# Kernel tuning notes

Measured on AMD Instinct MI355X. Metric: run time of the kernel, lower is better.

The kernel has to match this reference:

```python
import jax, jax.numpy as jnp
import numpy as np

N, E, G = 8192, 65536, 16          # nodes, edges, graphs
EMBED, HID, L = 512, 1024, 3       # embed_dim, hidden_dim, hidden_layers
NG, RBF_R = 50, 12.0               # num_gaussians, rbf_radius
AVG_LEN = 60.0
IN_DIM = 3 * EMBED


def _mlp_params(key, in_dim, hid, out_dim, n_layers):
    ks = jax.random.split(key, 6)
    s_in = 1.0 / np.sqrt(in_dim)
    s_h = 1.0 / np.sqrt(hid)
    return dict(
        in_w=jax.random.normal(ks[0], (in_dim, hid), jnp.float32) * s_in,
        in_b=jnp.zeros((hid,), jnp.float32),
        hid_w=jax.random.normal(ks[1], (n_layers, hid, hid), jnp.float32) * s_h,
        hid_b=jnp.zeros((n_layers, hid), jnp.float32),
        out_w=jax.random.normal(ks[2], (hid, out_dim), jnp.float32) * s_h,
        out_b=jnp.zeros((out_dim,), jnp.float32),
    )


def setup_inputs() -> dict:
    key = jax.random.key(0)
    k = jax.random.split(key, 8)
    x = jax.random.normal(k[0], (N, EMBED), jnp.float32)
    edge_index = jax.random.randint(k[1], (2, E), 0, N, dtype=jnp.int32)
    batch = jnp.sort(jax.random.randint(k[2], (N,), 0, G, dtype=jnp.int32))
    dist = jax.random.uniform(k[3], (E,), jnp.float32) * RBF_R
    v = jax.random.normal(k[4], (E, 3), jnp.float32)
    vec_hat = v / jnp.linalg.norm(v, axis=-1, keepdims=True)
    rbf_w = jax.random.normal(k[5], (NG, EMBED), jnp.float32) * (1.0 / np.sqrt(NG))
    rbf_b = jnp.zeros((EMBED,), jnp.float32)
    e = _mlp_params(k[6], IN_DIM, HID, 1, L)
    f = _mlp_params(k[7], IN_DIM, HID, 1, L)
    return dict(
        x=x, edge_index=edge_index, batch=batch, dist=dist, vec_hat=vec_hat,
        rbf_w=rbf_w, rbf_b=rbf_b,
        e_in_w=e['in_w'], e_in_b=e['in_b'], e_hid_w=e['hid_w'], e_hid_b=e['hid_b'], e_out_w=e['out_w'], e_out_b=e['out_b'],
        f_in_w=f['in_w'], f_in_b=f['in_b'], f_hid_w=f['hid_w'], f_hid_b=f['hid_b'], f_out_w=f['out_w'], f_out_b=f['out_b'],
    )


def _res_mlp(h_in, in_w, in_b, hid_w, hid_b, out_w, out_b):
    h = jax.nn.silu(h_in @ in_w + in_b)           # [E, HID]
    for i in range(L):                             # residual hidden blocks
        h = h + jax.nn.silu(h @ hid_w[i] + hid_b[i])
    return h @ out_w + out_b                       # [E, 1]


def _rbf(dist, rbf_w, rbf_b):
    offsets = jnp.linspace(0.0, RBF_R, NG)
    coeff = -0.5 / (offsets[1] - offsets[0]) ** 2
    g = jnp.exp(coeff * (dist[:, None] - offsets) ** 2)  # [E, NG]
    return g @ rbf_w + rbf_b                              # [E, EMBED]


def reference(x, edge_index, batch, dist, vec_hat,
              rbf_w, rbf_b,
              e_in_w, e_in_b, e_hid_w, e_hid_b, e_out_w, e_out_b,
              f_in_w, f_in_b, f_hid_w, f_hid_b, f_out_w, f_out_b):
    src, dst = edge_index[0], edge_index[1]
    rbf = _rbf(dist, rbf_w, rbf_b)                                 # [E, EMBED]
    inputs = jnp.concatenate([x[src], x[dst], rbf], axis=-1)       # [E, 3*EMBED]
    energy_pairs = _res_mlp(inputs, e_in_w, e_in_b, e_hid_w, e_hid_b, e_out_w, e_out_b)  # [E,1]
    force_pairs = _res_mlp(inputs, f_in_w, f_in_b, f_hid_w, f_hid_b, f_out_w, f_out_b) * vec_hat  # [E,3]
    energy = jax.ops.segment_sum(energy_pairs, batch[src], num_segments=G) / (AVG_LEN ** 2)  # [G,1]
    forces = jax.ops.segment_sum(force_pairs, src, num_segments=N) / AVG_LEN                 # [N,3]
    return energy, forces
```

## Files before the change

kernel.cpp:

```cpp
#include <hip/hip_runtime.h>
#include <math.h>

#define NUM_E 65536
#define NUM_N 8192
#define NUM_G 16
#define RBFR 12.0f

typedef unsigned short u16;
typedef _Float16 f16x8 __attribute__((ext_vector_type(8)));
typedef _Float16 f16x4 __attribute__((ext_vector_type(4)));
typedef float f32x4 __attribute__((ext_vector_type(4)));

#define TILE_F16 4096
#define L1SZ   1114112
#define HSZ    1048576
#define MSTRIDE 4259840

#define FU1  139264
#define FUHL 131072
#define FUPM (FU1 + 3 * FUHL)

#define GLD16(gp, lp) __builtin_amdgcn_global_load_lds( \
    (const __attribute__((address_space(1))) void*)(gp), \
    (__attribute__((address_space(3))) void*)(lp), 16, 0, 0)

#define VMW3()  asm volatile("s_waitcnt vmcnt(3)" ::: "memory")
#define VMW0()  asm volatile("s_waitcnt vmcnt(0)" ::: "memory")
#define BARX()  __builtin_amdgcn_s_barrier()

__global__ void wrbf_kernel(const float* __restrict__ rbf_w, const float* __restrict__ rbf_b,
                            const float* __restrict__ e_in_w, const float* __restrict__ e_in_b,
                            const float* __restrict__ f_in_w, const float* __restrict__ f_in_b,
                            float* __restrict__ wrbf_e, float* __restrict__ b1_e,
                            float* __restrict__ wrbf_f, float* __restrict__ b1_f) {
  int blk = blockIdx.x;
  int mlp = blk / 204;
  int rr = blk % 204;
  int row = rr >> 2;
  int ns = rr & 3;
  const float* in_w = mlp ? f_in_w : e_in_w;
  const float* in_b = mlp ? f_in_b : e_in_b;
  float* wrbf = mlp ? wrbf_f : wrbf_e;
  float* b1   = mlp ? b1_f : b1_e;
  __shared__ float vec[512];
  __shared__ float4 red[256];
  int tid = threadIdx.x;
  vec[tid]       = (row < 50) ? rbf_w[row * 512 + tid]       : rbf_b[tid];
  vec[tid + 256] = (row < 50) ? rbf_w[row * 512 + tid + 256] : rbf_b[tid + 256];
  __syncthreads();
  int q = tid >> 6, l = tid & 63;
  int n0 = ns * 256 + l * 4;
  float a0 = 0.f, a1 = 0.f, a2 = 0.f, a3 = 0.f;
#pragma unroll 4
  for (int c = q * 128; c < q * 128 + 128; ++c) {
    float4 wv = *(const float4*)&in_w[(size_t)(1024 + c) * 1024 + n0];
    float gv = vec[c];
    a0 += gv * wv.x; a1 += gv * wv.y; a2 += gv * wv.z; a3 += gv * wv.w;
  }
  red[tid] = float4{a0, a1, a2, a3};
  __syncthreads();
  if (q == 0) {
    float4 s0 = red[l], s1 = red[l + 64], s2 = red[l + 128], s3 = red[l + 192];
    float4 o = {s0.x + s1.x + s2.x + s3.x, s0.y + s1.y + s2.y + s3.y,
                s0.z + s1.z + s2.z + s3.z, s0.w + s1.w + s2.w + s3.w};
    if (row < 50) {
      *(float4*)&wrbf[row * 1024 + n0] = o;
    } else {
      o.x += in_b[n0]; o.y += in_b[n0 + 1]; o.z += in_b[n0 + 2]; o.w += in_b[n0 + 3];
      *(float4*)&b1[n0] = o;
    }
  }
}

__global__ void prep_kernel(const float* __restrict__ x, const float* __restrict__ dist,
                            u16* __restrict__ xh, u16* __restrict__ grbf) {
  int bid = blockIdx.x, tid = threadIdx.x;
  if (bid < 4096) {
    int i = bid * 256 + tid;
    float4 v = ((const float4*)x)[i];
    f16x4 h = {(_Float16)v.x, (_Float16)v.y, (_Float16)v.z, (_Float16)v.w};
    *(f16x4*)(xh + (size_t)i * 4) = h;
  } else {
    int u = (bid - 4096) * 256 + tid;
    int e = u >> 3, q = u & 7;
    const float delta = RBFR / 49.f;
    const float coeff = -0.5f / (delta * delta);
    float d = dist[e];
    f16x8 h;
#pragma unroll
    for (int j = 0; j < 8; ++j) {
      int gi = q * 8 + j;
      float dd = d - (float)gi * delta;
      float gg = (gi < 50) ? __expf(coeff * dd * dd) : 0.f;
      h[j] = (_Float16)gg;
    }
    *(f16x8*)(grbf + (size_t)u * 8) = h;
  }
}

__global__ void pack_gemm(const float* __restrict__ e_in_w, const float* __restrict__ e_hid_w,
                          const float* __restrict__ f_in_w, const float* __restrict__ f_hid_w,
                          const float* __restrict__ wrbf_e, const float* __restrict__ wrbf_f,
                          u16* __restrict__ wp) {
  __shared__ __align__(16) u16 tile[TILE_F16];
  int bid = blockIdx.x;
  int mlpi = (bid >= 1040) ? 1 : 0;
  int t = bid - mlpi * 1040;
  const float* in_w  = mlpi ? f_in_w : e_in_w;
  const float* hid_w = mlpi ? f_hid_w : e_hid_w;
  const float* wrbf  = mlpi ? wrbf_f : wrbf_e;
  int tid = threadIdx.x;
  int bnp, nhp, k0, lay = 0, is_l1;
  if (t < 272) {
    int grp = t / 34; int kt = t % 34;
    bnp = grp >> 1; nhp = grp & 1; k0 = kt * 32; is_l1 = 1;
  } else {
    int th = t - 272; lay = th >> 8; int t2 = th & 255;
    bnp = t2 >> 6; nhp = (t2 >> 5) & 1; k0 = (t2 & 31) * 32; is_l1 = 0;
  }
#pragma unroll
  for (int it = 0; it < 4; ++it) {
    int flat = it * 1024 + tid * 4;
    int k = flat >> 7;
    int nl4 = flat & 127;
    int n0 = bnp * 256 + ((nl4 >> 5) << 6) + nhp * 32 + (nl4 & 31);
    int kg = k0 + k;
    float4 v;
    if (is_l1) {
      if (kg < 1024)      v = *(const float4*)&in_w[(size_t)kg * 1024 + n0];
      else if (kg < 1074) v = *(const float4*)&wrbf[(size_t)(kg - 1024) * 1024 + n0];
      else                v = float4{0.f, 0.f, 0.f, 0.f};
    } else {
      v = *(const float4*)&hid_w[(size_t)((lay << 10) + kg) * 1024 + n0];
    }
#pragma unroll
    for (int c = 0; c < 4; ++c) {
      int nl = nl4 + c;
      int pos = nl * 32 + (((((k >> 3) ^ ((nl >> 1) & 3))) << 3) | (k & 7));
      _Float16 hf = (_Float16)(((const float*)&v)[c]);
      tile[pos] = __builtin_bit_cast(u16, hf);
    }
  }
  __syncthreads();
  u16* dst = wp + (size_t)mlpi * MSTRIDE + (size_t)t * TILE_F16;
#pragma unroll
  for (int i = 0; i < 2; ++i) {
    int off = (i * 256 + tid) * 8;
    *(f16x8*)(dst + off) = *(const f16x8*)(tile + off);
  }
}


#define STA(b, ah, kt) do { \
  const u16* _gp; \
  if (MODE == 1) { \
    int _off = ((kt) < 16) ? (osrc[ah] + (kt) * 32) \
             : (((kt) < 32) ? (odst[ah] + ((kt) - 16) * 32) : (ogr[ah] + ((kt) - 32) * 32)); \
    _gp = (((kt) < 32) ? hin : grbf) + _off; \
  } else { \
    _gp = hin + ((size_t)(rowb + atr + (ah) * 32) * 1024 + (kt) * 32 + akg * 8); \
  } \
  GLD16(_gp, (char*)&sm[b][ah][0] + wv * 1024); \
} while (0)

#define STB(b, kt) do { \
  const u16* _wt = wl + ((size_t)(bn * NKT + (kt))) * TILE_F16; \
  GLD16(_wt + wv * 512 + lane * 8, (char*)&sm[b][2][0] + wv * 1024); \
} while (0)

#define RDA(b, ah) do { \
  _Pragma("unroll") for (int _m = 0; _m < 2; ++_m) { \
    int _r = wm * 32 + _m * 16 + (lane & 15); \
    af[_m] = *(const f16x8*)&sm[b][ah][_r * 32 + ((((lane >> 4) ^ ((_r >> 1) & 3))) << 3)]; \
  } \
} while (0)

#define RDB(b) do { \
  _Pragma("unroll") for (int _n = 0; _n < 4; ++_n) { \
    int _c = wn * 64 + _n * 16 + (lane & 15); \
    bf[_n] = *(const f16x8*)&sm[b][2][_c * 32 + ((((lane >> 4) ^ ((_c >> 1) & 3))) << 3)]; \
  } \
} while (0)

#define PHM(ah) do { \
  __builtin_amdgcn_s_setprio(1); \
  _Pragma("unroll") for (int _m = 0; _m < 2; ++_m) \
    _Pragma("unroll") for (int _n = 0; _n < 4; ++_n) \
      acc[(ah) * 2 + _m][_n] = __builtin_amdgcn_mfma_f32_16x16x32_f16( \
          bf[_n], af[_m], acc[(ah) * 2 + _m][_n], 0, 0, 0); \
  __builtin_amdgcn_s_setprio(0); \
} while (0)

template<int NKT, int MODE>
__global__ __launch_bounds__(512, 4) void gemm8k(
    const u16* __restrict__ hinE, const u16* __restrict__ hinF,
    const u16* __restrict__ grbf, const int* __restrict__ eidx,
    const int* __restrict__ batch, const float* __restrict__ vhat,
    const u16* __restrict__ wp, size_t woff,
    const float* __restrict__ biasE, const float* __restrict__ biasF,
    u16* __restrict__ houtE, u16* __restrict__ houtF,
    const float* __restrict__ owE, const float* __restrict__ owF,
    const float* __restrict__ obE, const float* __restrict__ obF,
    float* __restrict__ out, int mstart) {
  __shared__ __align__(16) u16 sm[2][3][4096];
  __shared__ int s_src[256];
  __shared__ int s_dst[256];
  __shared__ float sred[256];
  __shared__ float sbins[16];
  const int tid = threadIdx.x;
  const int lane = tid & 63;
  const int wv = tid >> 6;
  const int wm = wv >> 1, wn = wv & 1;

  const int xcd = blockIdx.x & 7;
  const int r = blockIdx.x >> 3;
  const int bn = r & 7;
  const int mlp = (r >> 3) & 1;
  const int mt = (r >> 4) * 8 + xcd;

  const u16* hin = (MODE == 1) ? hinE : (mlp ? hinF : hinE);
  const u16* wl = wp + (size_t)mlp * MSTRIDE + woff;
  const float* bias = mlp ? biasF : biasE;
  u16* hout = mlp ? houtF : houtE;
  const int rowb = mt * 256;
  const int eg0 = mstart + rowb;
  const int bnp = bn >> 1, nhp = bn & 1;

  const int arl = wv * 16 + (lane >> 2);
  const int akg = (lane & 3) ^ ((arl >> 1) & 3);
  const int atr = ((arl >> 5) << 6) + (arl & 31);

  int osrc[2], odst[2], ogr[2];
  if (MODE == 1) {
    if (tid < 256) s_src[tid] = eidx[eg0 + tid];
    else s_dst[tid - 256] = eidx[NUM_E + eg0 + tid - 256];
    __syncthreads();
#pragma unroll
    for (int ah = 0; ah < 2; ++ah) {
      int tr = atr + ah * 32;
      osrc[ah] = s_src[tr] * 512 + akg * 8;
      odst[ah] = s_dst[tr] * 512 + akg * 8;
      ogr[ah]  = (eg0 + tr) * 64 + akg * 8;
    }
  }

  f32x4 acc[4][4];
#pragma unroll
  for (int m = 0; m < 4; ++m)
#pragma unroll
    for (int n = 0; n < 4; ++n)
#pragma unroll
      for (int i = 0; i < 4; ++i) acc[m][n][i] = 0.f;

  f16x8 af[2], bf[4];

  STA(0, 0, 0); STB(0, 0); STA(0, 1, 0);
  VMW0(); BARX();

  for (int t = 0; t < NKT - 1; ++t) {
    const int b = t & 1, nb = b ^ 1;
    STA(nb, 0, t + 1); STB(nb, t + 1); STA(nb, 1, t + 1);
    VMW3(); BARX();
    RDA(b, 0); RDB(b);
    PHM(0);
    RDA(b, 1);
    PHM(1);
    BARX();
  }
  {
    const int tb = (NKT - 1) & 1;
    VMW0(); BARX();
    RDA(tb, 0); RDB(tb);
    PHM(0);
    RDA(tb, 1);
    PHM(1);
  }

  if (MODE != 2) {
#pragma unroll
    for (int m = 0; m < 4; ++m) {
      int grow = rowb + wm * 64 + (m >> 1) * 32 + (m & 1) * 16 + (lane & 15);
#pragma unroll
      for (int n = 0; n < 4; ++n) {
        int c = wn * 64 + n * 16 + ((lane >> 4) << 2);
        int gn = bnp * 256 + ((c >> 5) << 6) + nhp * 32 + (c & 31);
        float4 bi = *(const float4*)&bias[gn];
        f16x4 o;
        if (MODE == 1) {
#pragma unroll
          for (int i = 0; i < 4; ++i) {
            float pre = acc[m][n][i] + ((const float*)&bi)[i];
            o[i] = (_Float16)(pre / (1.f + __expf(-pre)));
          }
        } else {
          f16x4 hp = *(const f16x4*)&hin[(size_t)grow * 1024 + gn];
#pragma unroll
          for (int i = 0; i < 4; ++i) {
            float pre = acc[m][n][i] + ((const float*)&bi)[i];
            o[i] = (_Float16)(pre / (1.f + __expf(-pre)) + (float)hp[i]);
          }
        }
        *(f16x4*)&hout[(size_t)grow * 1024 + gn] = o;
      }
    }
  } else {
    if (tid < 256) sred[tid] = 0.f;
    if (tid < 16) sbins[tid] = 0.f;
    __syncthreads();
    const float* ow = mlp ? owF : owE;
    float p[4];
#pragma unroll
    for (int m = 0; m < 4; ++m) p[m] = 0.f;
#pragma unroll
    for (int m = 0; m < 4; ++m) {
      int grow = rowb + wm * 64 + (m >> 1) * 32 + (m & 1) * 16 + (lane & 15);
#pragma unroll
      for (int n = 0; n < 4; ++n) {
        int c = wn * 64 + n * 16 + ((lane >> 4) << 2);
        int gn = bnp * 256 + ((c >> 5) << 6) + nhp * 32 + (c & 31);
        float4 bi = *(const float4*)&bias[gn];
        float4 wv4 = *(const float4*)&ow[gn];
        f16x4 hp = *(const f16x4*)&hin[(size_t)grow * 1024 + gn];
#pragma unroll
        for (int i = 0; i < 4; ++i) {
          float pre = acc[m][n][i] + ((const float*)&bi)[i];
          float val = pre / (1.f + __expf(-pre)) + (float)hp[i];
          p[m] += val * ((const float*)&wv4)[i];
        }
      }
    }
#pragma unroll
    for (int m = 0; m < 4; ++m) {
      p[m] += __shfl_down(p[m], 32, 64);
      p[m] += __shfl_down(p[m], 16, 64);
    }
    if ((lane >> 4) == 0) {
#pragma unroll
      for (int m = 0; m < 4; ++m)
        atomicAdd(&sred[wm * 64 + (m >> 1) * 32 + (m & 1) * 16 + lane], p[m]);
    }
    __syncthreads();
    if (tid < 256) {
      float s = sred[tid];
      int eg = eg0 + tid;
      int si = eidx[eg];
      if (mlp == 0) {
        float pv = s + ((bn == 0) ? obE[0] : 0.f);
        atomicAdd(&sbins[batch[si]], pv);
      } else {
        float pv = (s + ((bn == 0) ? obF[0] : 0.f)) * (1.f / 60.f);
        atomicAdd(&out[16 + si * 3 + 0], pv * vhat[(size_t)eg * 3 + 0]);
        atomicAdd(&out[16 + si * 3 + 1], pv * vhat[(size_t)eg * 3 + 1]);
        atomicAdd(&out[16 + si * 3 + 2], pv * vhat[(size_t)eg * 3 + 2]);
      }
    }
    __syncthreads();
    if (mlp == 0 && tid < 16) atomicAdd(&out[tid], sbins[tid] * (1.f / 3600.f));
  }
}

#define FSWZ(row, col) ((((row) * 1088) + (col)) ^ (((row) & 7) << 3))

__global__ void packF_kernel(const float* __restrict__ e_in_w, const float* __restrict__ e_hid_w,
                             const float* __restrict__ f_in_w, const float* __restrict__ f_hid_w,
                             const float* __restrict__ wrbf_e, const float* __restrict__ wrbf_f,
                             u16* __restrict__ wp) {
  int u = blockIdx.x * 256 + threadIdx.x;
  if (u >= 2 * FUPM) return;
  int m = (u >= FUPM) ? 1 : 0;
  int v = u - m * FUPM;
  const float* in_w  = m ? f_in_w : e_in_w;
  const float* hid_w = m ? f_hid_w : e_hid_w;
  const float* wrbf  = m ? wrbf_f : wrbf_e;
  int l = v & 63;
  int kb = (l >> 4) << 3;
  f16x8 vals;
  if (v < FU1) {
    int kt = v >> 12;
    int ntg = (v >> 6) & 63;
    int n = ntg * 16 + (l & 15);
    int k0 = kt * 32 + kb;
#pragma unroll
    for (int jj = 0; jj < 8; ++jj) {
      int k = k0 + jj;
      float f = (k < 1024) ? in_w[(size_t)k * 1024 + n]
              : ((k < 1074) ? wrbf[(k - 1024) * 1024 + n] : 0.f);
      vals[jj] = (_Float16)f;
    }
  } else {
    int vh = v - FU1;
    int lay = vh >> 17;
    int kt = (vh >> 12) & 31;
    int ntg = (vh >> 6) & 63;
    int n = ntg * 16 + (l & 15);
    int k0 = kt * 32 + kb;
#pragma unroll
    for (int jj = 0; jj < 8; ++jj)
      vals[jj] = (_Float16)hid_w[(size_t)((lay << 10) + k0 + jj) * 1024 + n];
  }
  *(f16x8*)(wp + (size_t)u * 8) = vals;
}

#define F_LOADB(buf, kt) do { \
  const u16* _wr = wl + ((size_t)((kt) * 64 + wave * 8) * 64 + lane) * 8; \
  _Pragma("unroll") \
  for (int _nt = 0; _nt < 8; ++_nt) buf[_nt] = *(const f16x8*)(_wr + (size_t)_nt * 512); \
} while (0)
#define F_LOADA(buf, kt) do { \
  const int _kb = (kt) * 32 + ((lane >> 4) << 3); \
  _Pragma("unroll") \
  for (int _r = 0; _r < 4; ++_r) buf[_r] = *(const f16x8*)&Alds[FSWZ(_r * 16 + (lane & 15), _kb)]; \
} while (0)
#define F_MFMAS(abuf, bbuf) do { \
  _Pragma("unroll") \
  for (int _nt = 0; _nt < 8; ++_nt) \
    _Pragma("unroll") \
    for (int _r = 0; _r < 4; ++_r) \
      acc[_r][_nt] = __builtin_amdgcn_mfma_f32_16x16x32_f16(abuf[_r], bbuf[_nt], acc[_r][_nt], 0, 0, 0); \
} while (0)

__global__ __launch_bounds__(512, 2) void fusedF_kernel(
    const float* __restrict__ x, const int* __restrict__ eidx,
    const int* __restrict__ batch, const float* __restrict__ dist,
    const float* __restrict__ vhat,
    const u16* __restrict__ wp,
    const float* __restrict__ b1_e, const float* __restrict__ b1_f,
    const float* __restrict__ e_hid_b, const float* __restrict__ f_hid_b,
    const float* __restrict__ e_out_w, const float* __restrict__ e_out_b,
    const float* __restrict__ f_out_w, const float* __restrict__ f_out_b,
    float* __restrict__ out) {
  __shared__ __align__(16) u16 Alds[64 * 1088];
  __shared__ float sow[1024];
  __shared__ float sbins[16];
  __shared__ int s_src[64];
  __shared__ int s_dst[64];
  __shared__ float s_dist[64];
  const int tid = threadIdx.x;
  const int lane = tid & 63;
  const int wave = tid >> 6;
  const int e0 = blockIdx.x * 64;
  if (tid < 16) sbins[tid] = 0.f;
  if (tid < 64) s_src[tid] = eidx[e0 + tid];
  if (tid >= 64 && tid < 128) s_dst[tid - 64] = eidx[NUM_E + e0 + tid - 64];
  if (tid >= 128 && tid < 192) s_dist[tid - 128] = dist[e0 + tid - 128];
  __syncthreads();
  const float delta = RBFR / 49.f;
  const float coeff = -0.5f / (delta * delta);
  for (int mlp = 0; mlp < 2; ++mlp) {
    for (int i = tid; i < 16384; i += 512) {
      int e = i >> 8;
      int part = (i >> 7) & 1;
      int q = i & 127;
      int nrow = part ? s_dst[e] : s_src[e];
      float4 v = ((const float4*)x)[(size_t)nrow * 128 + q];
      int col = part * 512 + q * 4;
      f16x4 hv = {(_Float16)v.x, (_Float16)v.y, (_Float16)v.z, (_Float16)v.w};
      *(f16x4*)&Alds[FSWZ(e, col)] = hv;
    }
    for (int i = tid; i < 4096; i += 512) {
      int e = i >> 6;
      int gi = i & 63;
      float d = s_dist[e] - (float)gi * delta;
      float g2 = (gi < 50) ? __expf(coeff * d * d) : 0.f;
      _Float16 hg = (_Float16)g2;
      Alds[FSWZ(e, 1024 + gi)] = __builtin_bit_cast(u16, hg);
    }
    __syncthreads();
    const u16* wp1 = wp + (size_t)mlp * FUPM * 8;
    const u16* wph = wp1 + (size_t)FU1 * 8;
    const float* b1 = mlp ? b1_f : b1_e;
    const float* hb = mlp ? f_hid_b : e_hid_b;
    for (int layer = 0; layer < 4; ++layer) {
      const int nkt = (layer == 0) ? 34 : 32;
      const u16* wl = (layer == 0) ? wp1 : (wph + (size_t)(layer - 1) * FUHL * 8);
      const float* bias = (layer == 0) ? b1 : (hb + (layer - 1) * 1024);
      f32x4 acc[4][8];
#pragma unroll
      for (int r = 0; r < 4; ++r)
#pragma unroll
        for (int nt = 0; nt < 8; ++nt)
#pragma unroll
          for (int i = 0; i < 4; ++i) acc[r][nt][i] = 0.f;
      f16x8 a0[4], a1[4], b0[8], b1r[8];
      F_LOADA(a0, 0); F_LOADB(b0, 0);
      F_LOADA(a1, 1); F_LOADB(b1r, 1);
      for (int kt = 0; kt < nkt; kt += 2) {
        F_MFMAS(a0, b0);
        if (kt + 2 < nkt) { F_LOADA(a0, kt + 2); F_LOADB(b0, kt + 2); }
        F_MFMAS(a1, b1r);
        if (kt + 3 < nkt) { F_LOADA(a1, kt + 3); F_LOADB(b1r, kt + 3); }
      }
      __syncthreads();
      float bia[8];
#pragma unroll
      for (int nt = 0; nt < 8; ++nt) bia[nt] = bias[wave * 128 + nt * 16 + (lane & 15)];
#pragma unroll
      for (int r = 0; r < 4; ++r) {
#pragma unroll
        for (int nt = 0; nt < 8; ++nt) {
#pragma unroll
          for (int i = 0; i < 4; ++i) {
            int row = r * 16 + ((lane >> 4) << 2) + i;
            int col = wave * 128 + nt * 16 + (lane & 15);
            float pre = acc[r][nt][i] + bia[nt];
            float val = pre / (1.f + __expf(-pre));
            int idx = FSWZ(row, col);
            if (layer > 0) {
              _Float16 oldh = __builtin_bit_cast(_Float16, Alds[idx]);
              val += (float)oldh;
            }
            _Float16 nh = (_Float16)val;
            Alds[idx] = __builtin_bit_cast(u16, nh);
          }
        }
      }
      __syncthreads();
    }
    const float* ow = mlp ? f_out_w : e_out_w;
    for (int i = tid; i < 1024; i += 512) sow[i] = ow[i];
    __syncthreads();
    {
      int e = tid >> 3;
      int part = tid & 7;
      float s = 0.f;
#pragma unroll
      for (int cc = 0; cc < 16; ++cc) {
        int col = part * 128 + cc * 8;
        f16x8 hv = *(const f16x8*)&Alds[FSWZ(e, col)];
#pragma unroll
        for (int q = 0; q < 8; ++q) s += (float)hv[q] * sow[col + q];
      }
      s += __shfl_down(s, 4, 8);
      s += __shfl_down(s, 2, 8);
      s += __shfl_down(s, 1, 8);
      if (part == 0) {
        if (mlp == 0) {
          float pp = s + e_out_b[0];
          int gg = batch[s_src[e]];
          atomicAdd(&sbins[gg], pp);
        } else {
          float pp = (s + f_out_b[0]) * (1.f / 60.f);
          int si = s_src[e];
          atomicAdd(&out[16 + si * 3 + 0], pp * vhat[(size_t)(e0 + e) * 3 + 0]);
          atomicAdd(&out[16 + si * 3 + 1], pp * vhat[(size_t)(e0 + e) * 3 + 1]);
          atomicAdd(&out[16 + si * 3 + 2], pp * vhat[(size_t)(e0 + e) * 3 + 2]);
        }
      }
    }
    __syncthreads();
  }
  if (tid < 16) atomicAdd(&out[tid], sbins[tid] * (1.f / 3600.f));
}

extern "C" void kernel_launch(void* const* d_in, const int* in_sizes, int n_in,
                              void* d_out, int out_size, void* d_ws, size_t ws_size,
                              hipStream_t stream) {
  (void)in_sizes; (void)n_in;
  const float* x      = (const float*)d_in[0];
  const int*   eidx   = (const int*)d_in[1];
  const int*   batch  = (const int*)d_in[2];
  const float* dist   = (const float*)d_in[3];
  const float* vhat   = (const float*)d_in[4];
  const float* rbf_w  = (const float*)d_in[5];
  const float* rbf_b  = (const float*)d_in[6];
  const float* e_in_w = (const float*)d_in[7];
  const float* e_in_b = (const float*)d_in[8];
  const float* e_hid_w = (const float*)d_in[9];
  const float* e_hid_b = (const float*)d_in[10];
  const float* e_out_w = (const float*)d_in[11];
  const float* e_out_b = (const float*)d_in[12];
  const float* f_in_w = (const float*)d_in[13];
  const float* f_in_b = (const float*)d_in[14];
  const float* f_hid_w = (const float*)d_in[15];
  const float* f_hid_b = (const float*)d_in[16];
  const float* f_out_w = (const float*)d_in[17];
  const float* f_out_b = (const float*)d_in[18];

  const size_t WP_BYTES = 17039360;
  u16* wp       = (u16*)d_ws;
  float* wrbf_e = (float*)((char*)d_ws + WP_BYTES);
  float* wrbf_f = wrbf_e + 50 * 1024;
  float* b1_e   = wrbf_f + 50 * 1024;
  float* b1_f   = b1_e + 1024;
  const size_t BASE = WP_BYTES + 409600 + 8192;
  u16* xh   = (u16*)((char*)d_ws + BASE);
  u16* grbf = (u16*)((char*)d_ws + BASE + 8388608);
  const size_t FIXED = BASE + 16777216;

  int nch = 0;
  for (int c = 1; c <= 8; c <<= 1) {
    size_t need = FIXED + 4 * (size_t)(NUM_E / c) * 1024 * sizeof(u16);
    if (need <= ws_size) { nch = c; break; }
  }

  hipMemsetAsync(d_out, 0, (size_t)out_size * sizeof(float), stream);
  wrbf_kernel<<<408, 256, 0, stream>>>(rbf_w, rbf_b, e_in_w, e_in_b, f_in_w, f_in_b,
                                       wrbf_e, b1_e, wrbf_f, b1_f);

  if (nch == 0) {
    packF_kernel<<<(2 * FUPM + 255) / 256, 256, 0, stream>>>(
        e_in_w, e_hid_w, f_in_w, f_hid_w, wrbf_e, wrbf_f, wp);
    fusedF_kernel<<<NUM_E / 64, 512, 0, stream>>>(x, eidx, batch, dist, vhat, wp,
                                                  b1_e, b1_f, e_hid_b, f_hid_b,
                                                  e_out_w, e_out_b, f_out_w, f_out_b,
                                                  (float*)d_out);
    return;
  }

  pack_gemm<<<2080, 256, 0, stream>>>(
      e_in_w, e_hid_w, f_in_w, f_hid_w, wrbf_e, wrbf_f, wp);
  prep_kernel<<<6144, 256, 0, stream>>>(x, dist, xh, grbf);

  const int Mchunk = NUM_E / nch;
  u16* hE0 = (u16*)((char*)d_ws + FIXED);
  u16* hE1 = hE0 + (size_t)Mchunk * 1024;
  u16* hF0 = hE1 + (size_t)Mchunk * 1024;
  u16* hF1 = hF0 + (size_t)Mchunk * 1024;
  float* out = (float*)d_out;

  for (int c = 0; c < nch; ++c) {
    int mstart = c * Mchunk;
    int grid = Mchunk / 16;
    gemm8k<34, 1><<<grid, 512, 0, stream>>>(
        xh, xh, grbf, eidx, batch, vhat, wp, 0,
        b1_e, b1_f, hE0, hF0, e_out_w, f_out_w, e_out_b, f_out_b, out, mstart);
    gemm8k<32, 0><<<grid, 512, 0, stream>>>(
        hE0, hF0, grbf, eidx, batch, vhat, wp, L1SZ,
        e_hid_b, f_hid_b, hE1, hF1, e_out_w, f_out_w, e_out_b, f_out_b, out, mstart);
    gemm8k<32, 0><<<grid, 512, 0, stream>>>(
        hE1, hF1, grbf, eidx, batch, vhat, wp, L1SZ + HSZ,
        e_hid_b + 1024, f_hid_b + 1024, hE0, hF0, e_out_w, f_out_w, e_out_b, f_out_b, out, mstart);
    gemm8k<32, 2><<<grid, 512, 0, stream>>>(
        hE0, hF0, grbf, eidx, batch, vhat, wp, L1SZ + 2 * HSZ,
        e_hid_b + 2048, f_hid_b + 2048, hE1, hF1, e_out_w, f_out_w, e_out_b, f_out_b, out, mstart);
  }
}
```

Baseline: 1.575 ms.

## Retile GEMM to 128x128x64 blocks with 256 threads and single-buffered LDS

```diff
diff --git a/kernel.cpp b/kernel.cpp
--- a/kernel.cpp
+++ b/kernel.cpp
@@ -11,7 +11,7 @@
 typedef _Float16 f16x4 __attribute__((ext_vector_type(4)));
 typedef float f32x4 __attribute__((ext_vector_type(4)));
 
-#define TILE_F16 4096
+#define TILE_F16 8192
 #define L1SZ   1114112
 #define HSZ    1048576
 #define MSTRIDE 4259840
@@ -23,10 +23,6 @@
 #define GLD16(gp, lp) __builtin_amdgcn_global_load_lds( \
     (const __attribute__((address_space(1))) void*)(gp), \
     (__attribute__((address_space(3))) void*)(lp), 16, 0, 0)
-
-#define VMW3()  asm volatile("s_waitcnt vmcnt(3)" ::: "memory")
-#define VMW0()  asm volatile("s_waitcnt vmcnt(0)" ::: "memory")
-#define BARX()  __builtin_amdgcn_s_barrier()
 
 __global__ void wrbf_kernel(const float* __restrict__ rbf_w, const float* __restrict__ rbf_b,
                             const float* __restrict__ e_in_w, const float* __restrict__ e_in_b,
@@ -104,26 +100,25 @@
                           u16* __restrict__ wp) {
   __shared__ __align__(16) u16 tile[TILE_F16];
   int bid = blockIdx.x;
-  int mlpi = (bid >= 1040) ? 1 : 0;
-  int t = bid - mlpi * 1040;
+  int mlpi = (bid >= 520) ? 1 : 0;
+  int t = bid - mlpi * 520;
   const float* in_w  = mlpi ? f_in_w : e_in_w;
   const float* hid_w = mlpi ? f_hid_w : e_hid_w;
   const float* wrbf  = mlpi ? wrbf_f : wrbf_e;
   int tid = threadIdx.x;
-  int bnp, nhp, k0, lay = 0, is_l1;
-  if (t < 272) {
-    int grp = t / 34; int kt = t % 34;
-    bnp = grp >> 1; nhp = grp & 1; k0 = kt * 32; is_l1 = 1;
+  int bn, k0, lay = 0, is_l1;
+  if (t < 136) {
+    bn = t / 17; k0 = (t % 17) * 64; is_l1 = 1;
   } else {
-    int th = t - 272; lay = th >> 8; int t2 = th & 255;
-    bnp = t2 >> 6; nhp = (t2 >> 5) & 1; k0 = (t2 & 31) * 32; is_l1 = 0;
-  }
-#pragma unroll
-  for (int it = 0; it < 4; ++it) {
+    int th = t - 136; lay = th >> 7; int r = th & 127;
+    bn = r >> 4; k0 = (r & 15) * 64; is_l1 = 0;
+  }
+#pragma unroll
+  for (int it = 0; it < 8; ++it) {
     int flat = it * 1024 + tid * 4;
     int k = flat >> 7;
     int nl4 = flat & 127;
-    int n0 = bnp * 256 + ((nl4 >> 5) << 6) + nhp * 32 + (nl4 & 31);
+    int n0 = bn * 128 + nl4;
     int kg = k0 + k;
     float4 v;
     if (is_l1) {
@@ -136,7 +131,7 @@
 #pragma unroll
     for (int c = 0; c < 4; ++c) {
       int nl = nl4 + c;
-      int pos = nl * 32 + (((((k >> 3) ^ ((nl >> 1) & 3))) << 3) | (k & 7));
+      int pos = nl * 64 + ((((k >> 3) ^ (nl & 7)) << 3) | (k & 7));
       _Float16 hf = (_Float16)(((const float*)&v)[c]);
       tile[pos] = __builtin_bit_cast(u16, hf);
     }
@@ -144,55 +139,64 @@
   __syncthreads();
   u16* dst = wp + (size_t)mlpi * MSTRIDE + (size_t)t * TILE_F16;
 #pragma unroll
-  for (int i = 0; i < 2; ++i) {
+  for (int i = 0; i < 4; ++i) {
     int off = (i * 256 + tid) * 8;
     *(f16x8*)(dst + off) = *(const f16x8*)(tile + off);
   }
 }
 
 
-#define STA(b, ah, kt) do { \
-  const u16* _gp; \
-  if (MODE == 1) { \
-    int _off = ((kt) < 16) ? (osrc[ah] + (kt) * 32) \
-             : (((kt) < 32) ? (odst[ah] + ((kt) - 16) * 32) : (ogr[ah] + ((kt) - 32) * 32)); \
-    _gp = (((kt) < 32) ? hin : grbf) + _off; \
-  } else { \
-    _gp = hin + ((size_t)(rowb + atr + (ah) * 32) * 1024 + (kt) * 32 + akg * 8); \
-  } \
-  GLD16(_gp, (char*)&sm[b][ah][0] + wv * 1024); \
-} while (0)
-
-#define STB(b, kt) do { \
-  const u16* _wt = wl + ((size_t)(bn * NKT + (kt))) * TILE_F16; \
-  GLD16(_wt + wv * 512 + lane * 8, (char*)&sm[b][2][0] + wv * 1024); \
-} while (0)
-
-#define RDA(b, ah) do { \
-  _Pragma("unroll") for (int _m = 0; _m < 2; ++_m) { \
-    int _r = wm * 32 + _m * 16 + (lane & 15); \
-    af[_m] = *(const f16x8*)&sm[b][ah][_r * 32 + ((((lane >> 4) ^ ((_r >> 1) & 3))) << 3)]; \
+#define STA(kt) do { \
+  _Pragma("unroll") for (int _u = 0; _u < 4; ++_u) { \
+    int _c = _u * 4 + wv; \
+    const u16* _gp; \
+    if (MODE == 1) { \
+      int _off = ((kt) < 8) ? (osrc[_u] + (kt) * 64) \
+               : (((kt) < 16) ? (odst[_u] + ((kt) - 8) * 64) : ogr[_u]); \
+      _gp = (((kt) < 16) ? hin : grbf) + _off; \
+    } else { \
+      int _row = _c * 8 + (lane >> 3); \
+      int _sw = ((lane & 7) ^ (_row & 7)) << 3; \
+      _gp = hin + ((size_t)(rowb + _row) * 1024 + (kt) * 64 + _sw); \
+    } \
+    GLD16(_gp, (char*)As + _c * 1024); \
   } \
 } while (0)
 
-#define RDB(b) do { \
-  _Pragma("unroll") for (int _n = 0; _n < 4; ++_n) { \
-    int _c = wn * 64 + _n * 16 + (lane & 15); \
-    bf[_n] = *(const f16x8*)&sm[b][2][_c * 32 + ((((lane >> 4) ^ ((_c >> 1) & 3))) << 3)]; \
+#define STB(kt) do { \
+  const u16* _wt = wl + ((size_t)(bn * NKT + (kt))) * TILE_F16; \
+  _Pragma("unroll") for (int _u = 0; _u < 4; ++_u) { \
+    int _c = _u * 4 + wv; \
+    GLD16(_wt + _c * 512 + lane * 8, (char*)Bs + _c * 1024); \
   } \
 } while (0)
 
-#define PHM(ah) do { \
+#define RDAB() do { \
+  _Pragma("unroll") for (int _ks = 0; _ks < 2; ++_ks) { \
+    int _kk = _ks * 4 + (lane >> 4); \
+    _Pragma("unroll") for (int _m = 0; _m < 4; ++_m) { \
+      int _r = wm * 64 + _m * 16 + (lane & 15); \
+      af[_m][_ks] = *(const f16x8*)&As[_r * 64 + ((_kk ^ (_r & 7)) << 3)]; \
+    } \
+    _Pragma("unroll") for (int _n = 0; _n < 4; ++_n) { \
+      int _cc = wn * 64 + _n * 16 + (lane & 15); \
+      bf[_n][_ks] = *(const f16x8*)&Bs[_cc * 64 + ((_kk ^ (_cc & 7)) << 3)]; \
+    } \
+  } \
+} while (0)
+
+#define MFMAS() do { \
   __builtin_amdgcn_s_setprio(1); \
-  _Pragma("unroll") for (int _m = 0; _m < 2; ++_m) \
-    _Pragma("unroll") for (int _n = 0; _n < 4; ++_n) \
-      acc[(ah) * 2 + _m][_n] = __builtin_amdgcn_mfma_f32_16x16x32_f16( \
-          bf[_n], af[_m], acc[(ah) * 2 + _m][_n], 0, 0, 0); \
+  _Pragma("unroll") for (int _ks = 0; _ks < 2; ++_ks) \
+    _Pragma("unroll") for (int _m = 0; _m < 4; ++_m) \
+      _Pragma("unroll") for (int _n = 0; _n < 4; ++_n) \
+        acc[_m][_n] = __builtin_amdgcn_mfma_f32_16x16x32_f16( \
+            bf[_n][_ks], af[_m][_ks], acc[_m][_n], 0, 0, 0); \
   __builtin_amdgcn_s_setprio(0); \
 } while (0)
 
 template<int NKT, int MODE>
-__global__ __launch_bounds__(512, 4) void gemm8k(
+__global__ __launch_bounds__(256, 3) void gemm8k(
     const u16* __restrict__ hinE, const u16* __restrict__ hinF,
     const u16* __restrict__ grbf, const int* __restrict__ eidx,
     const int* __restrict__ batch, const float* __restrict__ vhat,
@@ -202,10 +206,11 @@
     const float* __restrict__ owE, const float* __restrict__ owF,
     const float* __restrict__ obE, const float* __restrict__ obF,
     float* __restrict__ out, int mstart) {
-  __shared__ __align__(16) u16 sm[2][3][4096];
-  __shared__ int s_src[256];
-  __shared__ int s_dst[256];
-  __shared__ float sred[256];
+  __shared__ __align__(16) u16 As[128 * 64];
+  __shared__ __align__(16) u16 Bs[128 * 64];
+  __shared__ int s_src[128];
+  __shared__ int s_dst[128];
+  __shared__ float sred[128];
   __shared__ float sbins[16];
   const int tid = threadIdx.x;
   const int lane = tid & 63;
@@ -222,25 +227,23 @@
   const u16* wl = wp + (size_t)mlp * MSTRIDE + woff;
   const float* bias = mlp ? biasF : biasE;
   u16* hout = mlp ? houtF : houtE;
-  const int rowb = mt * 256;
+  const int rowb = mt * 128;
+  const int n0 = bn * 128;
   const int eg0 = mstart + rowb;
-  const int bnp = bn >> 1, nhp = bn & 1;
-
-  const int arl = wv * 16 + (lane >> 2);
-  const int akg = (lane & 3) ^ ((arl >> 1) & 3);
-  const int atr = ((arl >> 5) << 6) + (arl & 31);
-
-  int osrc[2], odst[2], ogr[2];
+
+  int osrc[4], odst[4], ogr[4];
   if (MODE == 1) {
-    if (tid < 256) s_src[tid] = eidx[eg0 + tid];
-    else s_dst[tid - 256] = eidx[NUM_E + eg0 + tid - 256];
-    __syncthreads();
-#pragma unroll
-    for (int ah = 0; ah < 2; ++ah) {
-      int tr = atr + ah * 32;
-      osrc[ah] = s_src[tr] * 512 + akg * 8;
-      odst[ah] = s_dst[tr] * 512 + akg * 8;
-      ogr[ah]  = (eg0 + tr) * 64 + akg * 8;
+    if (tid < 128) { s_src[tid] = eidx[eg0 + tid]; }
+    else { s_dst[tid - 128] = eidx[NUM_E + eg0 + tid - 128]; }
+    __syncthreads();
+#pragma unroll
+    for (int u = 0; u < 4; ++u) {
+      int c = u * 4 + wv;
+      int row = c * 8 + (lane >> 3);
+      int sw = ((lane & 7) ^ (row & 7)) << 3;
+      osrc[u] = s_src[row] * 512 + sw;
+      odst[u] = s_dst[row] * 512 + sw;
+      ogr[u]  = (eg0 + row) * 64 + sw;
     }
   }
 
@@ -252,38 +255,23 @@
 #pragma unroll
       for (int i = 0; i < 4; ++i) acc[m][n][i] = 0.f;
 
-  f16x8 af[2], bf[4];
-
-  STA(0, 0, 0); STB(0, 0); STA(0, 1, 0);
-  VMW0(); BARX();
-
-  for (int t = 0; t < NKT - 1; ++t) {
-    const int b = t & 1, nb = b ^ 1;
-    STA(nb, 0, t + 1); STB(nb, t + 1); STA(nb, 1, t + 1);
-    VMW3(); BARX();
-    RDA(b, 0); RDB(b);
-    PHM(0);
-    RDA(b, 1);
-    PHM(1);
-    BARX();
-  }
-  {
-    const int tb = (NKT - 1) & 1;
-    VMW0(); BARX();
-    RDA(tb, 0); RDB(tb);
-    PHM(0);
-    RDA(tb, 1);
-    PHM(1);
+  f16x8 af[4][2], bf[4][2];
+
+  for (int kt = 0; kt < NKT; ++kt) {
+    STA(kt); STB(kt);
+    __syncthreads();
+    RDAB();
+    MFMAS();
+    __syncthreads();
   }
 
   if (MODE != 2) {
 #pragma unroll
     for (int m = 0; m < 4; ++m) {
-      int grow = rowb + wm * 64 + (m >> 1) * 32 + (m & 1) * 16 + (lane & 15);
+      int grow = rowb + wm * 64 + m * 16 + (lane & 15);
 #pragma unroll
       for (int n = 0; n < 4; ++n) {
-        int c = wn * 64 + n * 16 + ((lane >> 4) << 2);
-        int gn = bnp * 256 + ((c >> 5) << 6) + nhp * 32 + (c & 31);
+        int gn = n0 + wn * 64 + n * 16 + ((lane >> 4) << 2);
         float4 bi = *(const float4*)&bias[gn];
         f16x4 o;
         if (MODE == 1) {
@@ -304,7 +292,7 @@
       }
     }
   } else {
-    if (tid < 256) sred[tid] = 0.f;
+    if (tid < 128) sred[tid] = 0.f;
     if (tid < 16) sbins[tid] = 0.f;
     __syncthreads();
     const float* ow = mlp ? owF : owE;
@@ -313,11 +301,10 @@
     for (int m = 0; m < 4; ++m) p[m] = 0.f;
 #pragma unroll
     for (int m = 0; m < 4; ++m) {
-      int grow = rowb + wm * 64 + (m >> 1) * 32 + (m & 1) * 16 + (lane & 15);
+      int grow = rowb + wm * 64 + m * 16 + (lane & 15);
 #pragma unroll
       for (int n = 0; n < 4; ++n) {
-        int c = wn * 64 + n * 16 + ((lane >> 4) << 2);
-        int gn = bnp * 256 + ((c >> 5) << 6) + nhp * 32 + (c & 31);
+        int gn = n0 + wn * 64 + n * 16 + ((lane >> 4) << 2);
         float4 bi = *(const float4*)&bias[gn];
         float4 wv4 = *(const float4*)&ow[gn];
         f16x4 hp = *(const f16x4*)&hin[(size_t)grow * 1024 + gn];
@@ -337,10 +324,10 @@
     if ((lane >> 4) == 0) {
 #pragma unroll
       for (int m = 0; m < 4; ++m)
-        atomicAdd(&sred[wm * 64 + (m >> 1) * 32 + (m & 1) * 16 + lane], p[m]);
-    }
-    __syncthreads();
-    if (tid < 256) {
+        atomicAdd(&sred[wm * 64 + m * 16 + (lane & 15)], p[m]);
+    }
+    __syncthreads();
+    if (tid < 128) {
       float s = sred[tid];
       int eg = eg0 + tid;
       int si = eidx[eg];
@@ -607,7 +594,7 @@
     return;
   }
 
-  pack_gemm<<<2080, 256, 0, stream>>>(
+  pack_gemm<<<1040, 256, 0, stream>>>(
       e_in_w, e_hid_w, f_in_w, f_hid_w, wrbf_e, wrbf_f, wp);
   prep_kernel<<<6144, 256, 0, stream>>>(x, dist, xh, grbf);
 
@@ -620,17 +607,17 @@
 
   for (int c = 0; c < nch; ++c) {
     int mstart = c * Mchunk;
-    int grid = Mchunk / 16;
-    gemm8k<34, 1><<<grid, 512, 0, stream>>>(
+    int grid = Mchunk / 8;
+    gemm8k<17, 1><<<grid, 256, 0, stream>>>(
         xh, xh, grbf, eidx, batch, vhat, wp, 0,
         b1_e, b1_f, hE0, hF0, e_out_w, f_out_w, e_out_b, f_out_b, out, mstart);
-    gemm8k<32, 0><<<grid, 512, 0, stream>>>(
+    gemm8k<16, 0><<<grid, 256, 0, stream>>>(
         hE0, hF0, grbf, eidx, batch, vhat, wp, L1SZ,
         e_hid_b, f_hid_b, hE1, hF1, e_out_w, f_out_w, e_out_b, f_out_b, out, mstart);
-    gemm8k<32, 0><<<grid, 512, 0, stream>>>(
+    gemm8k<16, 0><<<grid, 256, 0, stream>>>(
         hE1, hF1, grbf, eidx, batch, vhat, wp, L1SZ + HSZ,
         e_hid_b + 1024, f_hid_b + 1024, hE0, hF0, e_out_w, f_out_w, e_out_b, f_out_b, out, mstart);
-    gemm8k<32, 2><<<grid, 512, 0, stream>>>(
+    gemm8k<16, 2><<<grid, 256, 0, stream>>>(
         hE0, hF0, grbf, eidx, batch, vhat, wp, L1SZ + 2 * HSZ,
         e_hid_b + 2048, f_hid_b + 2048, hE1, hF1, e_out_w, f_out_w, e_out_b, f_out_b, out, mstart);
   }
```

Measured after the change: 1.506 ms. 4.4% less time.
